# Kernel tuning notes

Hardware: AMD Instinct MI355X
Metric: run time of the kernel (lower is better)

Reference implementation:

```python
import jax, jax.numpy as jnp
import numpy as np

H = 8   # num_heads
K = 7   # kernel_size


def setup_inputs() -> dict:
    key = jax.random.key(0)
    k1, k2, k3 = jax.random.split(key, 3)
    T, B, C = 2048, 16, 512
    x = jax.random.normal(k1, (T, B, C), dtype=jnp.float32)
    query = jax.random.normal(k2, (T, B, C), dtype=jnp.float32)
    W = jax.random.normal(k3, (C, H * K), dtype=jnp.float32) * 0.02
    return {"x": x, "query": query, "W": W}


def reference(x, query, W):
    T, B, C = x.shape
    R = C // H
    # per-position, per-head kernel weights: Dense(H*K) on query, no bias
    weight = jnp.einsum('tbc,cn->tbn', query, W).reshape(T * B * H, K)
    weight = jax.nn.softmax(weight, axis=-1)  # weight_softmax=True; dropout rate 0 is identity
    # TF extract_patches with SAME padding along T: total pad K-1, more on the bottom
    pad_before = (K - 1) // 2
    pad_after = K - 1 - pad_before
    x_pad = jnp.pad(x, ((pad_before, pad_after), (0, 0), (0, 0)))
    idx = jnp.arange(T)[:, None] + jnp.arange(K)[None, :]  # (T, K)
    patches = x_pad[idx]                      # (T, K, B, C)
    patches = jnp.transpose(patches, (0, 2, 1, 3))  # (T, B, K, C): TF depth order is (k, c)
    # Faithful to the source: flat (K*C) axis reinterpreted as (H, R, K)
    x_unfold = patches.reshape(T * B * H, R, K)
    out = jnp.einsum('nrk,nk->nr', x_unfold, weight)  # batched tiny matmul
    return out.reshape(T, B, C)
```

## Files before the change

kernel.cpp:

```cpp
#include <hip/hip_runtime.h>

#define T_DIM 2048
#define B_DIM 16
#define C_DIM 512
#define NW 56
#define ROWS (T_DIM * B_DIM)
#define SA 136

typedef __attribute__((ext_vector_type(8))) short short8;
typedef __attribute__((ext_vector_type(4))) short short4v;
typedef __attribute__((ext_vector_type(4))) float floatx4;

static __device__ __forceinline__ unsigned short f2bf(float x) {
    union { float f; unsigned u; } v; v.f = x;
    return (unsigned short)((v.u + 0x7FFFu + ((v.u >> 16) & 1u)) >> 16);
}

__global__ __launch_bounds__(256)
void weights_kernel(const float* __restrict__ q, const float* __restrict__ W,
                    float* __restrict__ wsw) {
    __shared__ union {
        struct { unsigned short A[64 * SA]; unsigned short Bt[64 * SA]; } s;
        float L[64 * 65];
    } u;

    const int tid  = threadIdx.x;
    const int lane = tid & 63;
    const int wv   = tid >> 6;
    const int r0   = blockIdx.x * 64;

    floatx4 acc[4];
#pragma unroll
    for (int nt = 0; nt < 4; ++nt) acc[nt] = (floatx4){0.f, 0.f, 0.f, 0.f};

    const int arow = tid >> 2;
    const int acol = (tid & 3) * 4;
    const int bk   = tid >> 1;
    const int bn0  = (tid & 1) * 28;
    const int m    = lane & 15, quad = lane >> 4;

    for (int kc = 0; kc < 512; kc += 128) {
        __syncthreads();
        const float* qp = q + (size_t)(r0 + arow) * C_DIM + kc + acol;
#pragma unroll
        for (int i = 0; i < 8; ++i) {
            const float4 v = *(const float4*)(qp + i * 16);
            short4v p;
            p.x = (short)f2bf(v.x); p.y = (short)f2bf(v.y);
            p.z = (short)f2bf(v.z); p.w = (short)f2bf(v.w);
            *(short4v*)(&u.s.A[arow * SA + acol + i * 16]) = p;
        }
        const float* wp = W + (size_t)(kc + bk) * NW + bn0;
#pragma unroll
        for (int j = 0; j < 28; ++j)
            u.s.Bt[(bn0 + j) * SA + bk] = f2bf(wp[j]);
        {
            const int n  = 56 + (tid & 7);
            const int k0 = (tid >> 3) * 4;
#pragma unroll
            for (int j = 0; j < 4; ++j) u.s.Bt[n * SA + k0 + j] = 0;
        }
        __syncthreads();
#pragma unroll
        for (int kt = 0; kt < 4; ++kt) {
            const short8 af = *(const short8*)(&u.s.A[(wv * 16 + m) * SA + kt * 32 + quad * 8]);
#pragma unroll
            for (int nt = 0; nt < 4; ++nt) {
                const short8 bf = *(const short8*)(&u.s.Bt[(nt * 16 + m) * SA + kt * 32 + quad * 8]);
                acc[nt] = __builtin_amdgcn_mfma_f32_16x16x32_bf16(af, bf, acc[nt], 0, 0, 0);
            }
        }
    }
    __syncthreads();
#pragma unroll
    for (int nt = 0; nt < 4; ++nt)
#pragma unroll
        for (int r = 0; r < 4; ++r)
            u.L[(wv * 16 + quad * 4 + r) * 65 + nt * 16 + m] = acc[nt][r];
    __syncthreads();
#pragma unroll
    for (int rep = 0; rep < 2; ++rep) {
        const int id  = tid + rep * 256;
        const int row = id >> 3, h = id & 7;
        const float* Lp = &u.L[row * 65 + h * 7];
        float mx = Lp[0];
#pragma unroll
        for (int k = 1; k < 7; ++k) mx = fmaxf(mx, Lp[k]);
        float e[7], s = 0.f;
#pragma unroll
        for (int k = 0; k < 7; ++k) { e[k] = __expf(Lp[k] - mx); s += e[k]; }
        const float inv = 1.0f / s;
        float* op = wsw + (size_t)(r0 + row) * NW + h * 7;
#pragma unroll
        for (int k = 0; k < 7; ++k) op[k] = e[k] * inv;
    }
}

static __device__ __forceinline__ int swz(int ba) { return ba ^ ((ba >> 2) & 0x70); }

__global__ __launch_bounds__(256)
void conv_kernel(const float* __restrict__ x, const float* __restrict__ wsw,
                 float* __restrict__ out) {
    __shared__ float xs[22 * 512];
    __shared__ float wt[16 * NW];

    const int tid = threadIdx.x;
    const int b   = blockIdx.x & 15;
    const int t0  = (blockIdx.x >> 4) * 16;

#pragma unroll
    for (int j = 0; j < 11; ++j) {
        const int idx = tid + j * 256;
        const int i   = idx >> 7;
        const int c   = (idx & 127) * 4;
        const int tp  = t0 + i - 3;
        float4 v = make_float4(0.f, 0.f, 0.f, 0.f);
        if (tp >= 0 && tp < T_DIM)
            v = *(const float4*)(x + (size_t)(tp * B_DIM + b) * C_DIM + c);
        *(float4*)((char*)xs + swz(idx * 16)) = v;
    }
    if (tid < 224) {
        const int tt = tid / 14, sg = tid % 14;
        const float* src = wsw + ((size_t)(t0 + tt) * B_DIM + b) * NW + sg * 4;
        *(float4*)(&wt[tt * NW + sg * 4]) = *(const float4*)src;
    }
    __syncthreads();

    const int lane   = tid & 63;
    const int wv     = tid >> 6;
    const int h      = lane >> 3;
    const int base_b = lane * 224;

#pragma unroll
    for (int qq = 0; qq < 4; ++qq) {
        const int tt = wv * 4 + qq;
        const int tb = tt * 2048 + base_b;
        float xv[56];
#pragma unroll
        for (int i = 0; i < 14; ++i)
            *(float4*)(&xv[i * 4]) = *(const float4*)((const char*)xs + swz(tb + i * 16));
        const float* wp = &wt[tt * NW + h * 7];
        float w[7];
#pragma unroll
        for (int k = 0; k < 7; ++k) w[k] = wp[k];
        float a[8];
#pragma unroll
        for (int r = 0; r < 8; ++r) {
            float s = xv[r * 7] * w[0];
#pragma unroll
            for (int k = 1; k < 7; ++k) s = fmaf(w[k], xv[r * 7 + k], s);
            a[r] = s;
        }
        float* orow = out + ((size_t)(t0 + tt) * B_DIM + b) * C_DIM + lane * 8;
        *(float4*)(orow)     = make_float4(a[0], a[1], a[2], a[3]);
        *(float4*)(orow + 4) = make_float4(a[4], a[5], a[6], a[7]);
    }
}

extern "C" void kernel_launch(void* const* d_in, const int* in_sizes, int n_in,
                              void* d_out, int out_size, void* d_ws, size_t ws_size,
                              hipStream_t stream) {
    const float* x = (const float*)d_in[0];
    const float* q = (const float*)d_in[1];
    const float* W = (const float*)d_in[2];
    float* out = (float*)d_out;
    float* wsw = (float*)d_ws;

    weights_kernel<<<ROWS / 64, 256, 0, stream>>>(q, W, wsw);
    conv_kernel<<<(T_DIM / 16) * B_DIM, 256, 0, stream>>>(x, wsw, out);
}
```

Measured before the change: 202.0 us.

## Fuse softmax-weight GEMM into conv kernel with bf16 LDS staging and prepacked W

Merges the weight-projection GEMM and softmax into the depthwise conv kernel, so each block computes its own 16x56 softmax weights via MFMA before applying them. W is prepacked into MFMA fragment order by a small kernel and held in registers. The x tile is stored in LDS as bf16 to halve LDS footprint and traffic. This removes the intermediate weights round-trip and a launch, but rounds x to bf16, which reduces output accuracy.

```diff
diff --git a/kernel.cpp b/kernel.cpp
--- a/kernel.cpp
+++ b/kernel.cpp
@@ -4,156 +4,169 @@
 #define B_DIM 16
 #define C_DIM 512
 #define NW 56
-#define ROWS (T_DIM * B_DIM)
-#define SA 136
+#define XS_BYTES (22 * 512 * 2)
+#define A_OFF    XS_BYTES
+#define WT_OFF   (XS_BYTES + 4160)
+#define LDS_TOTAL (XS_BYTES + 16384)
 
 typedef __attribute__((ext_vector_type(8))) short short8;
-typedef __attribute__((ext_vector_type(4))) short short4v;
 typedef __attribute__((ext_vector_type(4))) float floatx4;
 
 static __device__ __forceinline__ unsigned short f2bf(float x) {
     union { float f; unsigned u; } v; v.f = x;
     return (unsigned short)((v.u + 0x7FFFu + ((v.u >> 16) & 1u)) >> 16);
 }
+static __device__ __forceinline__ float bf_lo(unsigned u) {
+    union { unsigned u; float f; } c; c.u = u << 16; return c.f;
+}
+static __device__ __forceinline__ float bf_hi(unsigned u) {
+    union { unsigned u; float f; } c; c.u = u & 0xFFFF0000u; return c.f;
+}
+static __device__ __forceinline__ int swz(int a) { return a ^ ((a >> 3) & 0x70); }
 
 __global__ __launch_bounds__(256)
-void weights_kernel(const float* __restrict__ q, const float* __restrict__ W,
-                    float* __restrict__ wsw) {
-    __shared__ union {
-        struct { unsigned short A[64 * SA]; unsigned short Bt[64 * SA]; } s;
-        float L[64 * 65];
-    } u;
+void pack_w(const float* __restrict__ W, short8* __restrict__ Bg) {
+    const int g  = blockIdx.x * 256 + threadIdx.x;
+    const int ks = g >> 8;
+    const int nt = (g >> 6) & 3;
+    const int l  = g & 63;
+    const int n  = nt * 16 + (l & 15);
+    const int k0 = ks * 32 + ((l >> 4) & 3) * 8;
+    short8 o;
+#pragma unroll
+    for (int j = 0; j < 8; ++j) {
+        const float v = (n < NW) ? W[(size_t)(k0 + j) * NW + n] : 0.f;
+        o[j] = (short)f2bf(v);
+    }
+    Bg[g] = o;
+}
+
+__global__ __launch_bounds__(256)
+void fused_kernel(const float* __restrict__ x, const float* __restrict__ q,
+                  const short8* __restrict__ Bg, float* __restrict__ out) {
+    __shared__ __align__(16) char S[LDS_TOTAL];
 
     const int tid  = threadIdx.x;
     const int lane = tid & 63;
     const int wv   = tid >> 6;
-    const int r0   = blockIdx.x * 64;
+    const int b    = blockIdx.x & 15;
+    const int t0   = (blockIdx.x >> 4) * 16;
 
-    floatx4 acc[4];
+    const int rq = lane & 15;
+    const int qq = lane >> 4;
+    const float* qrow = q + ((size_t)(t0 + rq) * B_DIM + b) * C_DIM + qq * 8;
+    float4 qr[4][2];
 #pragma unroll
-    for (int nt = 0; nt < 4; ++nt) acc[nt] = (floatx4){0.f, 0.f, 0.f, 0.f};
-
-    const int arow = tid >> 2;
-    const int acol = (tid & 3) * 4;
-    const int bk   = tid >> 1;
-    const int bn0  = (tid & 1) * 28;
-    const int m    = lane & 15, quad = lane >> 4;
-
-    for (int kc = 0; kc < 512; kc += 128) {
-        __syncthreads();
-        const float* qp = q + (size_t)(r0 + arow) * C_DIM + kc + acol;
+    for (int s = 0; s < 4; ++s) {
+        const int ks = wv + s * 4;
+        qr[s][0] = *(const float4*)(qrow + ks * 32);
+        qr[s][1] = *(const float4*)(qrow + ks * 32 + 4);
+    }
+    short8 bfr[16];
 #pragma unroll
-        for (int i = 0; i < 8; ++i) {
-            const float4 v = *(const float4*)(qp + i * 16);
-            short4v p;
-            p.x = (short)f2bf(v.x); p.y = (short)f2bf(v.y);
-            p.z = (short)f2bf(v.z); p.w = (short)f2bf(v.w);
-            *(short4v*)(&u.s.A[arow * SA + acol + i * 16]) = p;
-        }
-        const float* wp = W + (size_t)(kc + bk) * NW + bn0;
-#pragma unroll
-        for (int j = 0; j < 28; ++j)
-            u.s.Bt[(bn0 + j) * SA + bk] = f2bf(wp[j]);
-        {
-            const int n  = 56 + (tid & 7);
-            const int k0 = (tid >> 3) * 4;
-#pragma unroll
-            for (int j = 0; j < 4; ++j) u.s.Bt[n * SA + k0 + j] = 0;
-        }
-        __syncthreads();
-#pragma unroll
-        for (int kt = 0; kt < 4; ++kt) {
-            const short8 af = *(const short8*)(&u.s.A[(wv * 16 + m) * SA + kt * 32 + quad * 8]);
-#pragma unroll
-            for (int nt = 0; nt < 4; ++nt) {
-                const short8 bf = *(const short8*)(&u.s.Bt[(nt * 16 + m) * SA + kt * 32 + quad * 8]);
-                acc[nt] = __builtin_amdgcn_mfma_f32_16x16x32_bf16(af, bf, acc[nt], 0, 0, 0);
-            }
-        }
-    }
-    __syncthreads();
-#pragma unroll
-    for (int nt = 0; nt < 4; ++nt)
-#pragma unroll
-        for (int r = 0; r < 4; ++r)
-            u.L[(wv * 16 + quad * 4 + r) * 65 + nt * 16 + m] = acc[nt][r];
-    __syncthreads();
-#pragma unroll
-    for (int rep = 0; rep < 2; ++rep) {
-        const int id  = tid + rep * 256;
-        const int row = id >> 3, h = id & 7;
-        const float* Lp = &u.L[row * 65 + h * 7];
-        float mx = Lp[0];
-#pragma unroll
-        for (int k = 1; k < 7; ++k) mx = fmaxf(mx, Lp[k]);
-        float e[7], s = 0.f;
-#pragma unroll
-        for (int k = 0; k < 7; ++k) { e[k] = __expf(Lp[k] - mx); s += e[k]; }
-        const float inv = 1.0f / s;
-        float* op = wsw + (size_t)(r0 + row) * NW + h * 7;
-#pragma unroll
-        for (int k = 0; k < 7; ++k) op[k] = e[k] * inv;
-    }
-}
-
-static __device__ __forceinline__ int swz(int ba) { return ba ^ ((ba >> 2) & 0x70); }
-
-__global__ __launch_bounds__(256)
-void conv_kernel(const float* __restrict__ x, const float* __restrict__ wsw,
-                 float* __restrict__ out) {
-    __shared__ float xs[22 * 512];
-    __shared__ float wt[16 * NW];
-
-    const int tid = threadIdx.x;
-    const int b   = blockIdx.x & 15;
-    const int t0  = (blockIdx.x >> 4) * 16;
-
+    for (int ks = 0; ks < 16; ++ks)
+        bfr[ks] = Bg[(ks * 4 + wv) * 64 + lane];
+    float4 xr[11];
 #pragma unroll
     for (int j = 0; j < 11; ++j) {
         const int idx = tid + j * 256;
         const int i   = idx >> 7;
         const int c   = (idx & 127) * 4;
         const int tp  = t0 + i - 3;
-        float4 v = make_float4(0.f, 0.f, 0.f, 0.f);
+        xr[j] = make_float4(0.f, 0.f, 0.f, 0.f);
         if (tp >= 0 && tp < T_DIM)
-            v = *(const float4*)(x + (size_t)(tp * B_DIM + b) * C_DIM + c);
-        *(float4*)((char*)xs + swz(idx * 16)) = v;
+            xr[j] = *(const float4*)(x + ((size_t)tp * B_DIM + b) * C_DIM + c);
     }
-    if (tid < 224) {
-        const int tt = tid / 14, sg = tid % 14;
-        const float* src = wsw + ((size_t)(t0 + tt) * B_DIM + b) * NW + sg * 4;
-        *(float4*)(&wt[tt * NW + sg * 4]) = *(const float4*)src;
+
+    short8* A8 = (short8*)(S + A_OFF);
+#pragma unroll
+    for (int s = 0; s < 4; ++s) {
+        const int ks = wv + s * 4;
+        short8 o;
+        o[0] = (short)f2bf(qr[s][0].x); o[1] = (short)f2bf(qr[s][0].y);
+        o[2] = (short)f2bf(qr[s][0].z); o[3] = (short)f2bf(qr[s][0].w);
+        o[4] = (short)f2bf(qr[s][1].x); o[5] = (short)f2bf(qr[s][1].y);
+        o[6] = (short)f2bf(qr[s][1].z); o[7] = (short)f2bf(qr[s][1].w);
+        A8[ks * 64 + lane] = o;
     }
     __syncthreads();
 
-    const int lane   = tid & 63;
-    const int wv     = tid >> 6;
-    const int h      = lane >> 3;
-    const int base_b = lane * 224;
+    floatx4 acc = (floatx4){0.f, 0.f, 0.f, 0.f};
+#pragma unroll
+    for (int ks = 0; ks < 16; ++ks) {
+        const short8 af = A8[ks * 64 + lane];
+        acc = __builtin_amdgcn_mfma_f32_16x16x32_bf16(af, bfr[ks], acc, 0, 0, 0);
+    }
 
+    char* XS = S;
 #pragma unroll
-    for (int qq = 0; qq < 4; ++qq) {
-        const int tt = wv * 4 + qq;
-        const int tb = tt * 2048 + base_b;
-        float xv[56];
+    for (int j = 0; j < 11; ++j) {
+        const int idx = tid + j * 256;
+        uint2 p;
+        p.x = (unsigned)f2bf(xr[j].x) | ((unsigned)f2bf(xr[j].y) << 16);
+        p.y = (unsigned)f2bf(xr[j].z) | ((unsigned)f2bf(xr[j].w) << 16);
+        const int a = idx * 8;
+        *(uint2*)(XS + swz(a)) = p;
+    }
+    __syncthreads();
+
+    float* L = (float*)(S + A_OFF);
+    const int m = lane & 15;
+    const int quad = lane >> 4;
 #pragma unroll
-        for (int i = 0; i < 14; ++i)
-            *(float4*)(&xv[i * 4]) = *(const float4*)((const char*)xs + swz(tb + i * 16));
-        const float* wp = &wt[tt * NW + h * 7];
+    for (int r = 0; r < 4; ++r)
+        L[(quad * 4 + r) * 65 + wv * 16 + m] = acc[r];
+    __syncthreads();
+
+    float* wt = (float*)(S + WT_OFF);
+    if (tid < 128) {
+        const int row = tid >> 3, h = tid & 7;
+        const float* Lp = L + row * 65 + h * 7;
+        float mx = Lp[0];
+#pragma unroll
+        for (int k = 1; k < 7; ++k) mx = fmaxf(mx, Lp[k]);
+        float e[7], sm = 0.f;
+#pragma unroll
+        for (int k = 0; k < 7; ++k) { e[k] = __expf(Lp[k] - mx); sm += e[k]; }
+        const float inv = 1.0f / sm;
+#pragma unroll
+        for (int k = 0; k < 7; ++k) wt[row * NW + h * 7 + k] = e[k] * inv;
+    }
+    __syncthreads();
+
+    const int h = lane >> 3;
+    const int base_b = lane * 112;
+#pragma unroll
+    for (int s = 0; s < 4; ++s) {
+        const int tt = wv * 4 + s;
+        const int tb = tt * 1024 + base_b;
+        uint4 xu[7];
+#pragma unroll
+        for (int i = 0; i < 7; ++i)
+            xu[i] = *(const uint4*)(XS + swz(tb + i * 16));
+        float xf[56];
+#pragma unroll
+        for (int i = 0; i < 7; ++i) {
+            xf[i * 8 + 0] = bf_lo(xu[i].x); xf[i * 8 + 1] = bf_hi(xu[i].x);
+            xf[i * 8 + 2] = bf_lo(xu[i].y); xf[i * 8 + 3] = bf_hi(xu[i].y);
+            xf[i * 8 + 4] = bf_lo(xu[i].z); xf[i * 8 + 5] = bf_hi(xu[i].z);
+            xf[i * 8 + 6] = bf_lo(xu[i].w); xf[i * 8 + 7] = bf_hi(xu[i].w);
+        }
+        const float* wp = wt + tt * NW + h * 7;
         float w[7];
 #pragma unroll
         for (int k = 0; k < 7; ++k) w[k] = wp[k];
-        float a[8];
+        float a8[8];
 #pragma unroll
         for (int r = 0; r < 8; ++r) {
-            float s = xv[r * 7] * w[0];
+            float sacc = xf[r * 7] * w[0];
 #pragma unroll
-            for (int k = 1; k < 7; ++k) s = fmaf(w[k], xv[r * 7 + k], s);
-            a[r] = s;
+            for (int k = 1; k < 7; ++k) sacc = fmaf(w[k], xf[r * 7 + k], sacc);
+            a8[r] = sacc;
         }
         float* orow = out + ((size_t)(t0 + tt) * B_DIM + b) * C_DIM + lane * 8;
-        *(float4*)(orow)     = make_float4(a[0], a[1], a[2], a[3]);
-        *(float4*)(orow + 4) = make_float4(a[4], a[5], a[6], a[7]);
+        *(float4*)(orow)     = make_float4(a8[0], a8[1], a8[2], a8[3]);
+        *(float4*)(orow + 4) = make_float4(a8[4], a8[5], a8[6], a8[7]);
     }
 }
 
@@ -164,8 +177,8 @@
     const float* q = (const float*)d_in[1];
     const float* W = (const float*)d_in[2];
     float* out = (float*)d_out;
-    float* wsw = (float*)d_ws;
+    short8* Bg = (short8*)d_ws;
 
-    weights_kernel<<<ROWS / 64, 256, 0, stream>>>(q, W, wsw);
-    conv_kernel<<<(T_DIM / 16) * B_DIM, 256, 0, stream>>>(x, wsw, out);
+    pack_w<<<16, 256, 0, stream>>>(W, Bg);
+    fused_kernel<<<(T_DIM / 16) * B_DIM, 256, 0, stream>>>(x, q, Bg, out);
 }
```

Result: faster. 174.5 us (-13.6%).
